# Optimization experiments

Measured on AMD Instinct MI355X. Metric: run time of the kernel, lower is better.

The kernel has to match this reference:

```python
import jax, jax.numpy as jnp
import numpy as np

HOPS = 2
BN_EPS = 1e-5


def _glorot(key, shape):
    fan_in = shape[-2]
    bound = 1.0 / np.sqrt(fan_in)
    return jax.random.uniform(key, shape, jnp.float32, -bound, bound)


def setup_inputs() -> dict:
    key = jax.random.key(0)
    ks = jax.random.split(key, 12)
    n, e = 50000, 800000
    in_c, hid, out_c = 128, 96, 64
    x = jax.random.normal(ks[0], (n, in_c), jnp.float32)
    edge_index = jax.random.randint(ks[1], (2, e), 0, n, jnp.int32)
    # MixHopLayer 0: hops+1 linears in_c -> hid (stacked)
    conv0_W = _glorot(ks[2], (HOPS + 1, in_c, hid))
    conv0_b = jnp.zeros((HOPS + 1, hid), jnp.float32)
    # MixHopLayer 1: hops+1 linears hid*(hops+1) -> out_c
    conv1_W = _glorot(ks[3], (HOPS + 1, hid * (HOPS + 1), out_c))
    conv1_b = jnp.zeros((HOPS + 1, out_c), jnp.float32)
    # BatchNorm1d(hid*(hops+1)) eval-mode params/buffers
    w = hid * (HOPS + 1)
    bn_gamma = jnp.ones((w,), jnp.float32)
    bn_beta = jnp.zeros((w,), jnp.float32)
    bn_mean = 0.1 * jax.random.normal(ks[4], (w,), jnp.float32)
    bn_var = jnp.ones((w,), jnp.float32) + 0.1 * jax.random.uniform(ks[5], (w,))
    # final projection out_c*(hops+1) -> out_c
    fp_W = _glorot(ks[6], (out_c * (HOPS + 1), out_c))
    fp_b = jnp.zeros((out_c,), jnp.float32)
    return dict(x=x, edge_index=edge_index, conv0_W=conv0_W, conv0_b=conv0_b,
                conv1_W=conv1_W, conv1_b=conv1_b, bn_gamma=bn_gamma, bn_beta=bn_beta,
                bn_mean=bn_mean, bn_var=bn_var, fp_W=fp_W, fp_b=fp_b)


def _gcn_norm(edge_index, n):
    # PyG gcn_norm with add_self_loops=True, improved=False, symmetric norm.
    row, col = edge_index[0], edge_index[1]
    loop = jnp.arange(n, dtype=edge_index.dtype)
    row = jnp.concatenate([row, loop])
    col = jnp.concatenate([col, loop])
    deg = jax.ops.segment_sum(jnp.ones_like(col, jnp.float32), col, num_segments=n)
    dinv = jnp.where(deg > 0, jax.lax.rsqrt(deg), 0.0)
    w = dinv[row] * dinv[col]
    return row, col, w


def _spmm_adj_t(row, col, w, x, n):
    # adj_t = SparseTensor(row=col, col=row, value=w): out[col] += w * x[row]
    return jax.ops.segment_sum(w[:, None] * x[row], col, num_segments=n)


def _mixhop_layer(x, W, b, row, col, w, n):
    xs = [x @ W[0] + b[0]]
    for j in range(1, HOPS + 1):
        xj = x @ W[j] + b[j]
        for _ in range(j):
            xj = _spmm_adj_t(row, col, w, xj, n)
        xs.append(xj)
    return jnp.concatenate(xs, axis=1)


def reference(x, edge_index, conv0_W, conv0_b, conv1_W, conv1_b,
              bn_gamma, bn_beta, bn_mean, bn_var, fp_W, fp_b):
    n = x.shape[0]
    row, col, w = _gcn_norm(edge_index, n)
    h = _mixhop_layer(x, conv0_W, conv0_b, row, col, w, n)
    # BatchNorm1d (eval) + ReLU; dropout is identity in eval
    h = bn_gamma * (h - bn_mean) * jax.lax.rsqrt(bn_var + BN_EPS) + bn_beta
    h = jax.nn.relu(h)
    h = _mixhop_layer(h, conv1_W, conv1_b, row, col, w, n)
    return h @ fp_W + fp_b
```

## Files before the change

### kernel.cpp

```cpp
#include <hip/hip_runtime.h>

#define IN_C 128
#define HID 96
#define OUT_C 64
#define W0C 288
#define W1C 192
#define CAP 5120
#define EPB 4096

typedef __bf16 bf16x8v __attribute__((ext_vector_type(8)));
typedef float  f32x4v  __attribute__((ext_vector_type(4)));


__global__ void k_zero(int* __restrict__ p, int n) {
    int i = blockIdx.x * blockDim.x + threadIdx.x;
    if (i < n) p[i] = 0;
}

__global__ void k_count(const int* __restrict__ col, int* __restrict__ counts, int e) {
    int i = blockIdx.x * blockDim.x + threadIdx.x;
    if (i < e) atomicAdd(&counts[col[i]], 1);
}

__global__ void k_block_sum(const int* __restrict__ counts, int* __restrict__ bsums,
                            float* __restrict__ dinv, int n) {
    __shared__ int s[256];
    int i = blockIdx.x * 256 + threadIdx.x;
    int v = (i < n) ? counts[i] : 0;
    if (i < n) dinv[i] = rsqrtf((float)(v + 1));
    s[threadIdx.x] = v;
    __syncthreads();
    for (int off = 128; off > 0; off >>= 1) {
        if (threadIdx.x < (unsigned)off) s[threadIdx.x] += s[threadIdx.x + off];
        __syncthreads();
    }
    if (threadIdx.x == 0) bsums[blockIdx.x] = s[0];
}

__global__ void k_scan_bsums(int* __restrict__ bsums, int nb) {
    __shared__ int s[256];
    int v = ((int)threadIdx.x < nb) ? bsums[threadIdx.x] : 0;
    s[threadIdx.x] = v;
    __syncthreads();
    for (int off = 1; off < 256; off <<= 1) {
        int t = ((int)threadIdx.x >= off) ? s[threadIdx.x - off] : 0;
        __syncthreads();
        s[threadIdx.x] += t;
        __syncthreads();
    }
    if ((int)threadIdx.x < nb) bsums[threadIdx.x] = s[threadIdx.x] - v;
}

__global__ void k_row_ptr(const int* __restrict__ counts, const int* __restrict__ boffs,
                          int* __restrict__ row_ptr, int n) {
    __shared__ int s[256];
    int i = blockIdx.x * 256 + threadIdx.x;
    int v = (i < n) ? counts[i] : 0;
    s[threadIdx.x] = v;
    __syncthreads();
    for (int off = 1; off < 256; off <<= 1) {
        int t = ((int)threadIdx.x >= off) ? s[threadIdx.x - off] : 0;
        __syncthreads();
        s[threadIdx.x] += t;
        __syncthreads();
    }
    if (i < n) {
        row_ptr[i] = boffs[blockIdx.x] + s[threadIdx.x] - v;
        if (i == n - 1) row_ptr[n] = boffs[blockIdx.x] + s[threadIdx.x];
    }
}

__global__ __launch_bounds__(256) void k_binscatter(
        const int* __restrict__ row, const int* __restrict__ col,
        const int* __restrict__ row_ptr, int* __restrict__ bcur ,
        int2* __restrict__ binned, int e) {
    __shared__ int hist[256];
    __shared__ int base[256];
    int tid = threadIdx.x;
    int e0 = blockIdx.x * EPB;
    int cnt = min(EPB, e - e0);
    hist[tid] = 0;
    __syncthreads();
    int rr[16], cc[16], rk[16];
#pragma unroll
    for (int k = 0; k < 16; k++) {
        int idx = tid + k * 256;
        if (idx < cnt) {
            rr[k] = row[e0 + idx];
            cc[k] = col[e0 + idx];
            rk[k] = atomicAdd(&hist[cc[k] >> 8], 1);
        }
    }
    __syncthreads();
    {
        int h = hist[tid];
        if (h > 0) base[tid] = atomicAdd(&bcur[tid * 16], h);
    }
    __syncthreads();
#pragma unroll
    for (int k = 0; k < 16; k++) {
        int idx = tid + k * 256;
        if (idx < cnt) {
            int b = cc[k] >> 8;
            binned[row_ptr[b << 8] + base[b] + rk[k]] = make_int2(rr[k], cc[k]);
        }
    }
}

__global__ __launch_bounds__(256) void k_bucket_sort(
        const int2* __restrict__ binned, const int* __restrict__ row_ptr,
        const float* __restrict__ dinv,
        int* __restrict__ csr_src, float* __restrict__ csr_w,
        float* __restrict__ arow, int n) {
    __shared__ int   s_src[CAP];
    __shared__ int   s_col[CAP];
    __shared__ int   s_ofs[256];
    __shared__ int   lcur[256];
    __shared__ float s_a[256];
    int tid = threadIdx.x;
    int node0 = blockIdx.x << 8;
    int nodeEnd = min(node0 + 256, n);
    int base = row_ptr[node0];
    int end  = row_ptr[nodeEnd];
    int cnt  = end - base;

    lcur[tid] = 0;
    __syncthreads();
    for (int t = tid; t < cnt; t += 256) {
        atomicAdd(&lcur[binned[base + t].x >> 8], 1);
    }
    __syncthreads();
    {
        int v = lcur[tid];
        s_ofs[tid] = v;
        __syncthreads();
        for (int o = 1; o < 256; o <<= 1) {
            int u = (tid >= o) ? s_ofs[tid - o] : 0;
            __syncthreads();
            s_ofs[tid] += u;
            __syncthreads();
        }
        lcur[tid] = s_ofs[tid] - v;
    }
    __syncthreads();
    for (int t = tid; t < cnt; t += 256) {
        int2 rc = binned[base + t];
        int pos = atomicAdd(&lcur[rc.x >> 8], 1);
        if (pos < CAP) {
            s_src[pos] = rc.x;
            s_col[pos] = rc.y;
        }
    }
    __syncthreads();
    {
        int node = node0 + tid;
        s_ofs[tid] = (node < n) ? (row_ptr[node] - base) : cnt;
        lcur[tid] = 0;
        s_a[tid] = 0.f;
    }
    __syncthreads();
    int lim = min(cnt, CAP);
    for (int t = tid; t < lim; t += 256) {
        int r = s_src[t], c = s_col[t];
        int local = c - node0;
        int pos = s_ofs[local] + atomicAdd(&lcur[local], 1);
        float wv = dinv[r] * dinv[c];
        csr_src[base + pos] = r;
        csr_w[base + pos]   = wv;
        atomicAdd(&s_a[local], wv);
    }
    __syncthreads();
    {
        int node = node0 + tid;
        if (node < n) {
            float d = dinv[node];
            arow[node] = s_a[tid] + d * d;
        }
    }
}


__global__ void k_cvt_bf16(const float* __restrict__ src, __bf16* __restrict__ dst, int n8) {
    int i = blockIdx.x * blockDim.x + threadIdx.x;
    if (i >= n8) return;
    bf16x8v o;
#pragma unroll
    for (int q = 0; q < 8; q++) o[q] = (__bf16)src[i * 8 + q];
    *(bf16x8v*)(dst + (size_t)i * 8) = o;
}

__global__ void k_prep_all(const float* __restrict__ W0, const float* __restrict__ W1,
                           const float* __restrict__ Wf,
                           const float* __restrict__ gamma, const float* __restrict__ beta,
                           const float* __restrict__ mean, const float* __restrict__ var,
                           __bf16* __restrict__ w0t, __bf16* __restrict__ w1t,
                           __bf16* __restrict__ wft,
                           float* __restrict__ scale, float* __restrict__ shift) {
    const int T0 = 3 * IN_C * HID;
    const int T1 = 3 * W0C * OUT_C;
    const int T2 = W1C * OUT_C;
    int i = blockIdx.x * blockDim.x + threadIdx.x;
    if (i < T0) {
        int kn = IN_C * HID;
        int j = i / kn, r = i % kn;
        int k = r / HID, nn = r % HID;
        w0t[(size_t)j * kn + (size_t)nn * IN_C + k] = (__bf16)W0[i];
    } else if (i < T0 + T1) {
        int ii = i - T0;
        int kn = W0C * OUT_C;
        int j = ii / kn, r = ii % kn;
        int k = r / OUT_C, nn = r % OUT_C;
        w1t[(size_t)j * kn + (size_t)nn * W0C + k] = (__bf16)W1[ii];
    } else if (i < T0 + T1 + T2) {
        int ii = i - T0 - T1;
        int k = ii / OUT_C, nn = ii % OUT_C;
        wft[(size_t)nn * W1C + k] = (__bf16)Wf[ii];
    } else if (i < T0 + T1 + T2 + W0C) {
        int ii = i - T0 - T1 - T2;
        float s = gamma[ii] * rsqrtf(var[ii] + 1e-5f);
        scale[ii] = s;
        shift[ii] = beta[ii] - mean[ii] * s;
    }
}


__global__ __launch_bounds__(256) void k_mf_l0a(
        const __bf16* __restrict__ xb, const __bf16* __restrict__ w0t ,
        const float* __restrict__ bias ,
        __bf16* __restrict__ h,
        const float* __restrict__ scale, const float* __restrict__ shift, int M) {
    const int RS = 104;
    __shared__ __bf16 tile[128 * RS];
    int tid = threadIdx.x;
    int wave = tid >> 6, lane = tid & 63;
    int ln = lane & 15, quad = lane >> 4;
    int rowBase = blockIdx.x * 128;
    int waveRow = wave * 16;
    f32x4v acc[2][6];
#pragma unroll
    for (int u = 0; u < 2; u++)
#pragma unroll
        for (int t = 0; t < 6; t++) acc[u][t] = (f32x4v){0.f, 0.f, 0.f, 0.f};
    const __bf16* arow0 = xb + (size_t)(rowBase + waveRow + ln) * IN_C + quad * 8;
    const __bf16* arow1 = arow0 + (size_t)64 * IN_C;
#pragma unroll
    for (int k = 0; k < 4; k++) {
        bf16x8v a0 = *(const bf16x8v*)(arow0 + k * 32);
        bf16x8v a1 = *(const bf16x8v*)(arow1 + k * 32);
#pragma unroll
        for (int c = 0; c < 6; c++) {
            bf16x8v b = *(const bf16x8v*)(w0t + (size_t)(c * 16 + ln) * IN_C + k * 32 + quad * 8);
            acc[0][c] = __builtin_amdgcn_mfma_f32_16x16x32_bf16(a0, b, acc[0][c], 0, 0, 0);
            acc[1][c] = __builtin_amdgcn_mfma_f32_16x16x32_bf16(a1, b, acc[1][c], 0, 0, 0);
        }
    }
#pragma unroll
    for (int u = 0; u < 2; u++)
#pragma unroll
        for (int r = 0; r < 4; r++) {
            int lr = u * 64 + waveRow + quad * 4 + r;
#pragma unroll
            for (int c = 0; c < 6; c++) {
                int col = c * 16 + ln;
                float v = acc[u][c][r] + bias[col];
                v = fmaxf(v * scale[col] + shift[col], 0.f);
                tile[lr * RS + col] = (__bf16)v;
            }
        }
    __syncthreads();
#pragma unroll
    for (int s = 0; s < 6; s++) {
        int idx = tid + s * 256;
        int r = idx / 12, c8 = idx % 12;
        int grow = rowBase + r;
        if (grow < M)
            *(bf16x8v*)(h + (size_t)grow * W0C + c8 * 8) =
                *(const bf16x8v*)(tile + r * RS + c8 * 8);
    }
}

__global__ __launch_bounds__(256) void k_mf_l0b(
        const __bf16* __restrict__ s1, const __bf16* __restrict__ w0t,
        const float* __restrict__ bias , const float* __restrict__ arow,
        __bf16* __restrict__ h, __bf16* __restrict__ tp,
        const float* __restrict__ scale, const float* __restrict__ shift, int M) {
    const int RS = 104;
    __shared__ __bf16 tile[128 * RS];
    int tid = threadIdx.x;
    int wave = tid >> 6, lane = tid & 63;
    int ln = lane & 15, quad = lane >> 4;
    int rowBase = blockIdx.x * 128;
    int waveRow = wave * 16;
    const __bf16* w1p = w0t + (size_t)1 * HID * IN_C;
    const __bf16* w2p = w0t + (size_t)2 * HID * IN_C;
    f32x4v acc[2][2][6];
#pragma unroll
    for (int j = 0; j < 2; j++)
#pragma unroll
        for (int u = 0; u < 2; u++)
#pragma unroll
            for (int t = 0; t < 6; t++) acc[j][u][t] = (f32x4v){0.f, 0.f, 0.f, 0.f};
    const __bf16* arow0 = s1 + (size_t)(rowBase + waveRow + ln) * IN_C + quad * 8;
    const __bf16* arow1 = arow0 + (size_t)64 * IN_C;
#pragma unroll
    for (int k = 0; k < 4; k++) {
        bf16x8v a0 = *(const bf16x8v*)(arow0 + k * 32);
        bf16x8v a1 = *(const bf16x8v*)(arow1 + k * 32);
#pragma unroll
        for (int c = 0; c < 6; c++) {
            bf16x8v b1 = *(const bf16x8v*)(w1p + (size_t)(c * 16 + ln) * IN_C + k * 32 + quad * 8);
            bf16x8v b2 = *(const bf16x8v*)(w2p + (size_t)(c * 16 + ln) * IN_C + k * 32 + quad * 8);
            acc[0][0][c] = __builtin_amdgcn_mfma_f32_16x16x32_bf16(a0, b1, acc[0][0][c], 0, 0, 0);
            acc[0][1][c] = __builtin_amdgcn_mfma_f32_16x16x32_bf16(a1, b1, acc[0][1][c], 0, 0, 0);
            acc[1][0][c] = __builtin_amdgcn_mfma_f32_16x16x32_bf16(a0, b2, acc[1][0][c], 0, 0, 0);
            acc[1][1][c] = __builtin_amdgcn_mfma_f32_16x16x32_bf16(a1, b2, acc[1][1][c], 0, 0, 0);
        }
    }
    float avs[2][4];
#pragma unroll
    for (int u = 0; u < 2; u++)
#pragma unroll
        for (int r = 0; r < 4; r++)
            avs[u][r] = arow[rowBase + u * 64 + waveRow + quad * 4 + r];
#pragma unroll
    for (int jj = 0; jj < 2; jj++) {
        const float* bj = bias + (jj + 1) * HID;
#pragma unroll
        for (int u = 0; u < 2; u++)
#pragma unroll
            for (int r = 0; r < 4; r++) {
                int lr = u * 64 + waveRow + quad * 4 + r;
                float av = avs[u][r];
#pragma unroll
                for (int c = 0; c < 6; c++) {
                    int col = c * 16 + ln;
                    float v = acc[jj][u][c][r] + av * bj[col];
                    if (jj == 0) v = fmaxf(v * scale[HID + col] + shift[HID + col], 0.f);
                    tile[lr * RS + col] = (__bf16)v;
                }
            }
        __syncthreads();
#pragma unroll
        for (int s = 0; s < 6; s++) {
            int idx = tid + s * 256;
            int r = idx / 12, c8 = idx % 12;
            int grow = rowBase + r;
            if (grow < M) {
                __bf16* dst = (jj == 0) ? (h + (size_t)grow * W0C + HID)
                                        : (tp + (size_t)grow * HID);
                *(bf16x8v*)(dst + c8 * 8) = *(const bf16x8v*)(tile + r * RS + c8 * 8);
            }
        }
        __syncthreads();
    }
}

__global__ __launch_bounds__(256) void k_mf_l1m(
        const __bf16* __restrict__ hb, const __bf16* __restrict__ w1t ,
        const float* __restrict__ bias ,
        __bf16* __restrict__ g, __bf16* __restrict__ u12, int M) {
    const int RS = 72;
    __shared__ __bf16 tile[128 * RS];
    int tid = threadIdx.x;
    int wave = tid >> 6, lane = tid & 63;
    int ln = lane & 15, quad = lane >> 4;
    int rowBase = blockIdx.x * 128;
    int waveRow = wave * 16;
    f32x4v acc[3][2][4];
#pragma unroll
    for (int j = 0; j < 3; j++)
#pragma unroll
        for (int u = 0; u < 2; u++)
#pragma unroll
            for (int t = 0; t < 4; t++) acc[j][u][t] = (f32x4v){0.f, 0.f, 0.f, 0.f};
    const __bf16* arow0 = hb + (size_t)(rowBase + waveRow + ln) * W0C + quad * 8;
    const __bf16* arow1 = arow0 + (size_t)64 * W0C;
#pragma unroll
    for (int k = 0; k < 9; k++) {
        bf16x8v a0 = *(const bf16x8v*)(arow0 + k * 32);
        bf16x8v a1 = *(const bf16x8v*)(arow1 + k * 32);
#pragma unroll
        for (int c = 0; c < 4; c++) {
#pragma unroll
            for (int j = 0; j < 3; j++) {
                bf16x8v b = *(const bf16x8v*)(w1t + (size_t)j * OUT_C * W0C +
                                              (size_t)(c * 16 + ln) * W0C + k * 32 + quad * 8);
                acc[j][0][c] = __builtin_amdgcn_mfma_f32_16x16x32_bf16(a0, b, acc[j][0][c], 0, 0, 0);
                acc[j][1][c] = __builtin_amdgcn_mfma_f32_16x16x32_bf16(a1, b, acc[j][1][c], 0, 0, 0);
            }
        }
    }
#pragma unroll
    for (int j = 0; j < 3; j++) {
        const float* bj = bias + j * OUT_C;
#pragma unroll
        for (int u = 0; u < 2; u++)
#pragma unroll
            for (int r = 0; r < 4; r++) {
                int lr = u * 64 + waveRow + quad * 4 + r;
#pragma unroll
                for (int c = 0; c < 4; c++) {
                    int col = c * 16 + ln;
                    tile[lr * RS + col] = (__bf16)(acc[j][u][c][r] + bj[col]);
                }
            }
        __syncthreads();
        __bf16* dst = (j == 0) ? g : u12;
        int ld = (j == 0) ? W1C : 128;
        int c0 = (j == 2) ? OUT_C : 0;
#pragma unroll
        for (int s = 0; s < 4; s++) {
            int idx = tid + s * 256;
            int r = idx / 8, c8 = idx % 8;
            int grow = rowBase + r;
            if (grow < M)
                *(bf16x8v*)(dst + (size_t)grow * ld + c0 + c8 * 8) =
                    *(const bf16x8v*)(tile + r * RS + c8 * 8);
        }
        __syncthreads();
    }
}

__global__ __launch_bounds__(256) void k_mf_fin(
        const __bf16* __restrict__ gb, const __bf16* __restrict__ wft ,
        const float* __restrict__ bias, float* __restrict__ out, int M) {
    const int RS = 68;
    __shared__ float tile[128 * RS];
    int tid = threadIdx.x;
    int wave = tid >> 6, lane = tid & 63;
    int ln = lane & 15, quad = lane >> 4;
    int rowBase = blockIdx.x * 128;
    int waveRow = wave * 16;
    f32x4v acc[2][4];
#pragma unroll
    for (int u = 0; u < 2; u++)
#pragma unroll
        for (int t = 0; t < 4; t++) acc[u][t] = (f32x4v){0.f, 0.f, 0.f, 0.f};
    const __bf16* arow0 = gb + (size_t)(rowBase + waveRow + ln) * W1C + quad * 8;
    const __bf16* arow1 = arow0 + (size_t)64 * W1C;
#pragma unroll
    for (int k = 0; k < 6; k++) {
        bf16x8v a0 = *(const bf16x8v*)(arow0 + k * 32);
        bf16x8v a1 = *(const bf16x8v*)(arow1 + k * 32);
#pragma unroll
        for (int c = 0; c < 4; c++) {
            bf16x8v b = *(const bf16x8v*)(wft + (size_t)(c * 16 + ln) * W1C + k * 32 + quad * 8);
            acc[0][c] = __builtin_amdgcn_mfma_f32_16x16x32_bf16(a0, b, acc[0][c], 0, 0, 0);
            acc[1][c] = __builtin_amdgcn_mfma_f32_16x16x32_bf16(a1, b, acc[1][c], 0, 0, 0);
        }
    }
#pragma unroll
    for (int u = 0; u < 2; u++)
#pragma unroll
        for (int r = 0; r < 4; r++) {
            int lr = u * 64 + waveRow + quad * 4 + r;
#pragma unroll
            for (int c = 0; c < 4; c++) {
                int col = c * 16 + ln;
                tile[lr * RS + col] = acc[u][c][r] + bias[col];
            }
        }
    __syncthreads();
#pragma unroll
    for (int s = 0; s < 8; s++) {
        int idx = tid + s * 256;
        int r = idx / 16, c4 = idx % 16;
        int grow = rowBase + r;
        if (grow < M)
            *(float4*)(out + (size_t)grow * OUT_C + c4 * 4) =
                *(const float4*)(tile + r * RS + c4 * 4);
    }
}

template <int C8, int NPB, bool BNRELU>
__global__ void k_spmm(const __bf16* __restrict__ xin, int ldx,
                       __bf16* __restrict__ xout, int ldo,
                       const int* __restrict__ row_ptr, const int* __restrict__ counts,
                       const int* __restrict__ csr_src, const float* __restrict__ csr_w,
                       const float* __restrict__ dinv, int n,
                       const float* __restrict__ scale, const float* __restrict__ shift,
                       int chan0) {
    int c8 = threadIdx.x % C8;
    int nl = threadIdx.x / C8;
    int node = blockIdx.x * NPB + nl;
    if (node >= n) return;
    float di = dinv[node];
    float lw = di * di;
    float acc[8];
    {
        bf16x8v v = *(const bf16x8v*)(xin + (size_t)node * ldx + c8 * 8);
#pragma unroll
        for (int q = 0; q < 8; q++) acc[q] = lw * (float)v[q];
    }
    int start = row_ptr[node];
    int cnt = counts[node];
    int k = 0;
    for (; k + 4 <= cnt; k += 4) {
        int s0 = csr_src[start + k + 0], s1 = csr_src[start + k + 1];
        int s2 = csr_src[start + k + 2], s3 = csr_src[start + k + 3];
        float w0 = csr_w[start + k + 0], w1 = csr_w[start + k + 1];
        float w2 = csr_w[start + k + 2], w3 = csr_w[start + k + 3];
        bf16x8v v0 = *(const bf16x8v*)(xin + (size_t)s0 * ldx + c8 * 8);
        bf16x8v v1 = *(const bf16x8v*)(xin + (size_t)s1 * ldx + c8 * 8);
        bf16x8v v2 = *(const bf16x8v*)(xin + (size_t)s2 * ldx + c8 * 8);
        bf16x8v v3 = *(const bf16x8v*)(xin + (size_t)s3 * ldx + c8 * 8);
#pragma unroll
        for (int q = 0; q < 8; q++)
            acc[q] += w0 * (float)v0[q] + w1 * (float)v1[q] +
                      w2 * (float)v2[q] + w3 * (float)v3[q];
    }
    for (; k < cnt; k++) {
        int src = csr_src[start + k];
        float w = csr_w[start + k];
        bf16x8v xv = *(const bf16x8v*)(xin + (size_t)src * ldx + c8 * 8);
#pragma unroll
        for (int q = 0; q < 8; q++) acc[q] += w * (float)xv[q];
    }
    bf16x8v o;
#pragma unroll
    for (int q = 0; q < 8; q++) {
        float v = acc[q];
        if (BNRELU) {
            int ch = chan0 + c8 * 8 + q;
            v = fmaxf(v * scale[ch] + shift[ch], 0.f);
        }
        o[q] = (__bf16)v;
    }
    *(bf16x8v*)(xout + (size_t)node * ldo + c8 * 8) = o;
}

template <int C8, int SPLIT, int NPB, bool BNA, bool BNB>
__global__ void k_spmm2(const __bf16* __restrict__ xin, int ldx,
                        __bf16* __restrict__ dstA, int ldA, int chanA,
                        __bf16* __restrict__ dstB, int ldB, int chanB,
                        const int* __restrict__ row_ptr, const int* __restrict__ counts,
                        const int* __restrict__ csr_src, const float* __restrict__ csr_w,
                        const float* __restrict__ dinv, int n,
                        const float* __restrict__ scale, const float* __restrict__ shift) {
    int c8 = threadIdx.x % C8;
    int nl = threadIdx.x / C8;
    int node = blockIdx.x * NPB + nl;
    if (node >= n) return;
    float di = dinv[node];
    float lw = di * di;
    float acc[8];
    {
        bf16x8v v = *(const bf16x8v*)(xin + (size_t)node * ldx + c8 * 8);
#pragma unroll
        for (int q = 0; q < 8; q++) acc[q] = lw * (float)v[q];
    }
    int start = row_ptr[node];
    int cnt = counts[node];
    int k = 0;
    for (; k + 4 <= cnt; k += 4) {
        int s0 = csr_src[start + k + 0], s1 = csr_src[start + k + 1];
        int s2 = csr_src[start + k + 2], s3 = csr_src[start + k + 3];
        float w0 = csr_w[start + k + 0], w1 = csr_w[start + k + 1];
        float w2 = csr_w[start + k + 2], w3 = csr_w[start + k + 3];
        bf16x8v v0 = *(const bf16x8v*)(xin + (size_t)s0 * ldx + c8 * 8);
        bf16x8v v1 = *(const bf16x8v*)(xin + (size_t)s1 * ldx + c8 * 8);
        bf16x8v v2 = *(const bf16x8v*)(xin + (size_t)s2 * ldx + c8 * 8);
        bf16x8v v3 = *(const bf16x8v*)(xin + (size_t)s3 * ldx + c8 * 8);
#pragma unroll
        for (int q = 0; q < 8; q++)
            acc[q] += w0 * (float)v0[q] + w1 * (float)v1[q] +
                      w2 * (float)v2[q] + w3 * (float)v3[q];
    }
    for (; k < cnt; k++) {
        int src = csr_src[start + k];
        float w = csr_w[start + k];
        bf16x8v xv = *(const bf16x8v*)(xin + (size_t)src * ldx + c8 * 8);
#pragma unroll
        for (int q = 0; q < 8; q++) acc[q] += w * (float)xv[q];
    }
    bool isA = c8 < SPLIT;
    __bf16* dst = isA ? dstA : dstB;
    int ld   = isA ? ldA : ldB;
    int lc8  = isA ? c8 : c8 - SPLIT;
    int chan = isA ? chanA : chanB;
    bool bn  = isA ? BNA : BNB;
    bf16x8v o;
#pragma unroll
    for (int q = 0; q < 8; q++) {
        float v = acc[q];
        if (bn) {
            int ch = chan + lc8 * 8 + q;
            v = fmaxf(v * scale[ch] + shift[ch], 0.f);
        }
        o[q] = (__bf16)v;
    }
    *(bf16x8v*)(dst + (size_t)node * ld + lc8 * 8) = o;
}


extern "C" void kernel_launch(void* const* d_in, const int* in_sizes, int n_in,
                              void* d_out, int out_size, void* d_ws, size_t ws_size,
                              hipStream_t stream) {
    const int n = in_sizes[0] / IN_C;
    const int e = in_sizes[1] / 2;

    const float* x    = (const float*)d_in[0];
    const int*   ei   = (const int*)d_in[1];
    const float* W0   = (const float*)d_in[2];
    const float* b0   = (const float*)d_in[3];
    const float* W1   = (const float*)d_in[4];
    const float* b1   = (const float*)d_in[5];
    const float* bn_g = (const float*)d_in[6];
    const float* bn_b = (const float*)d_in[7];
    const float* bn_m = (const float*)d_in[8];
    const float* bn_v = (const float*)d_in[9];
    const float* Wf   = (const float*)d_in[10];
    const float* bf   = (const float*)d_in[11];
    float* out = (float*)d_out;

    const int* e_row = ei;
    const int* e_col = ei + e;

    char* ws = (char*)d_ws;
    size_t off = 0;
    auto alloc = [&](size_t bytes) -> void* {
        void* p = ws + off;
        off += (bytes + 255) & ~(size_t)255;
        return p;
    };
    const int NP = n + 128;
    int*    counts  = (int*)alloc((size_t)(n + 256 * 16) * 4);
    int*    bcur    = counts + n;
    int*    row_ptr = (int*)alloc((size_t)(n + 1) * 4);
    int*    bsums   = (int*)alloc(256 * 4);
    float*  dinv    = (float*)alloc((size_t)n * 4);
    float*  arow    = (float*)alloc((size_t)NP * 4);
    int2*   binned  = (int2*)alloc((size_t)e * 8);
    int*    csr_src = (int*)alloc((size_t)e * 4);
    float*  csr_w   = (float*)alloc((size_t)e * 4);
    float*  bnscale = (float*)alloc(W0C * 4);
    float*  bnshift = (float*)alloc(W0C * 4);
    __bf16* xb  = (__bf16*)alloc((size_t)NP * IN_C * 2);
    __bf16* w0t = (__bf16*)alloc((size_t)3 * HID * IN_C * 2);
    __bf16* w1t = (__bf16*)alloc((size_t)3 * OUT_C * W0C * 2);
    __bf16* wft = (__bf16*)alloc((size_t)OUT_C * W1C * 2);
    __bf16* s1  = (__bf16*)alloc((size_t)NP * 128 * 2);
    __bf16* tp  = (__bf16*)alloc((size_t)NP * HID * 2);
    __bf16* h   = (__bf16*)alloc((size_t)NP * W0C * 2);
    __bf16* g   = (__bf16*)alloc((size_t)NP * W1C * 2);
    __bf16* u12 = s1;
    __bf16* up  = tp;

    const int TB = 256;
    int nb = (n + 255) / 256;

    k_zero<<<dim3((n + 256 * 16 + TB - 1) / TB), dim3(TB), 0, stream>>>(counts, n + 256 * 16);
    k_count<<<dim3((e + TB - 1) / TB), dim3(TB), 0, stream>>>(e_col, counts, e);
    k_block_sum<<<dim3(nb), dim3(256), 0, stream>>>(counts, bsums, dinv, n);
    k_scan_bsums<<<dim3(1), dim3(256), 0, stream>>>(bsums, nb);
    k_row_ptr<<<dim3(nb), dim3(256), 0, stream>>>(counts, bsums, row_ptr, n);
    k_binscatter<<<dim3((e + EPB - 1) / EPB), dim3(256), 0, stream>>>(e_row, e_col, row_ptr,
                                                                      bcur, binned, e);
    k_bucket_sort<<<dim3(nb), dim3(256), 0, stream>>>(binned, row_ptr, dinv,
                                                      csr_src, csr_w, arow, n);

    k_cvt_bf16<<<dim3((n * IN_C / 8 + TB - 1) / TB), dim3(TB), 0, stream>>>(x, xb, n * IN_C / 8);
    int ptotal = 3 * IN_C * HID + 3 * W0C * OUT_C + W1C * OUT_C + W0C;
    k_prep_all<<<dim3((ptotal + TB - 1) / TB), dim3(TB), 0, stream>>>(
        W0, W1, Wf, bn_g, bn_b, bn_m, bn_v, w0t, w1t, wft, bnscale, bnshift);

    dim3 g128((n + 127) / 128);

    k_mf_l0a<<<g128, dim3(256), 0, stream>>>(xb, w0t, b0, h, bnscale, bnshift, n);
    k_spmm<16, 16, false><<<dim3((n + 15) / 16), dim3(256), 0, stream>>>(
        xb, IN_C, s1, 128, row_ptr, counts, csr_src, csr_w, dinv, n,
        nullptr, nullptr, 0);
    k_mf_l0b<<<g128, dim3(256), 0, stream>>>(s1, w0t, b0, arow, h, tp, bnscale, bnshift, n);
    k_spmm<12, 16, true><<<dim3((n + 15) / 16), dim3(192), 0, stream>>>(
        tp, HID, h + 2 * HID, W0C, row_ptr, counts, csr_src, csr_w, dinv, n,
        bnscale, bnshift, 2 * HID);

    k_mf_l1m<<<g128, dim3(256), 0, stream>>>(h, w1t, b1, g, u12, n);

    k_spmm2<16, 8, 16, false, false><<<dim3((n + 15) / 16), dim3(256), 0, stream>>>(
        u12, 128, g + OUT_C, W1C, 0, up, OUT_C, 0,
        row_ptr, counts, csr_src, csr_w, dinv, n, nullptr, nullptr);
    k_spmm<8, 32, false><<<dim3((n + 31) / 32), dim3(256), 0, stream>>>(
        up, OUT_C, g + 2 * OUT_C, W1C, row_ptr, counts, csr_src, csr_w, dinv, n,
        nullptr, nullptr, 0);

    k_mf_fin<<<g128, dim3(256), 0, stream>>>(g, wft, bf, out, n);
}
```

Measured before the change: 354.4 us.

## Merge prep kernels, overlap edge counting with layer-0 GEMM, shrink GEMM tiles

Three prep launches (x-to-bf16 conversion, weight transpose/BN fold, counter zeroing) become one kernel that dispatches on block index. The edge-degree atomic count now runs as extra blocks inside the first layer-0 GEMM launch, so the two overlap and launch overhead drops. The l0b and l1m GEMMs move from 128-row to 64-row tiles, which doubles the block count and halves per-thread accumulators, trading B-operand reuse for occupancy. Reordering puts the l0a GEMM before CSR construction; it depends only on xb and the prep outputs, so this stays valid.

```diff
diff --git a/kernel.cpp b/kernel.cpp
--- a/kernel.cpp
+++ b/kernel.cpp
@@ -11,16 +11,6 @@
 typedef __bf16 bf16x8v __attribute__((ext_vector_type(8)));
 typedef float  f32x4v  __attribute__((ext_vector_type(4)));
 
-
-__global__ void k_zero(int* __restrict__ p, int n) {
-    int i = blockIdx.x * blockDim.x + threadIdx.x;
-    if (i < n) p[i] = 0;
-}
-
-__global__ void k_count(const int* __restrict__ col, int* __restrict__ counts, int e) {
-    int i = blockIdx.x * blockDim.x + threadIdx.x;
-    if (i < e) atomicAdd(&counts[col[i]], 1);
-}
 
 __global__ void k_block_sum(const int* __restrict__ counts, int* __restrict__ bsums,
                             float* __restrict__ dinv, int n) {
@@ -179,58 +169,70 @@
     }
 }
 
-
-__global__ void k_cvt_bf16(const float* __restrict__ src, __bf16* __restrict__ dst, int n8) {
-    int i = blockIdx.x * blockDim.x + threadIdx.x;
-    if (i >= n8) return;
-    bf16x8v o;
-#pragma unroll
-    for (int q = 0; q < 8; q++) o[q] = (__bf16)src[i * 8 + q];
-    *(bf16x8v*)(dst + (size_t)i * 8) = o;
-}
-
-__global__ void k_prep_all(const float* __restrict__ W0, const float* __restrict__ W1,
-                           const float* __restrict__ Wf,
-                           const float* __restrict__ gamma, const float* __restrict__ beta,
-                           const float* __restrict__ mean, const float* __restrict__ var,
-                           __bf16* __restrict__ w0t, __bf16* __restrict__ w1t,
-                           __bf16* __restrict__ wft,
-                           float* __restrict__ scale, float* __restrict__ shift) {
-    const int T0 = 3 * IN_C * HID;
-    const int T1 = 3 * W0C * OUT_C;
-    const int T2 = W1C * OUT_C;
-    int i = blockIdx.x * blockDim.x + threadIdx.x;
-    if (i < T0) {
-        int kn = IN_C * HID;
-        int j = i / kn, r = i % kn;
-        int k = r / HID, nn = r % HID;
-        w0t[(size_t)j * kn + (size_t)nn * IN_C + k] = (__bf16)W0[i];
-    } else if (i < T0 + T1) {
-        int ii = i - T0;
-        int kn = W0C * OUT_C;
-        int j = ii / kn, r = ii % kn;
-        int k = r / OUT_C, nn = r % OUT_C;
-        w1t[(size_t)j * kn + (size_t)nn * W0C + k] = (__bf16)W1[ii];
-    } else if (i < T0 + T1 + T2) {
-        int ii = i - T0 - T1;
-        int k = ii / OUT_C, nn = ii % OUT_C;
-        wft[(size_t)nn * W1C + k] = (__bf16)Wf[ii];
-    } else if (i < T0 + T1 + T2 + W0C) {
-        int ii = i - T0 - T1 - T2;
-        float s = gamma[ii] * rsqrtf(var[ii] + 1e-5f);
-        scale[ii] = s;
-        shift[ii] = beta[ii] - mean[ii] * s;
-    }
-}
-
-
-__global__ __launch_bounds__(256) void k_mf_l0a(
+__global__ void k_combo_prep(const float* __restrict__ x, __bf16* __restrict__ xb, int n8,
+                             const float* __restrict__ W0, const float* __restrict__ W1,
+                             const float* __restrict__ Wf,
+                             const float* __restrict__ gamma, const float* __restrict__ beta,
+                             const float* __restrict__ mean, const float* __restrict__ var,
+                             __bf16* __restrict__ w0t, __bf16* __restrict__ w1t,
+                             __bf16* __restrict__ wft,
+                             float* __restrict__ scale, float* __restrict__ shift,
+                             int* __restrict__ zp, int nz,
+                             int CB, int PB) {
+    int b = blockIdx.x;
+    if (b < CB) {
+        int i = b * 256 + threadIdx.x;
+        if (i >= n8) return;
+        bf16x8v o;
+#pragma unroll
+        for (int q = 0; q < 8; q++) o[q] = (__bf16)x[i * 8 + q];
+        *(bf16x8v*)(xb + (size_t)i * 8) = o;
+    } else if (b < CB + PB) {
+        const int T0 = 3 * IN_C * HID;
+        const int T1 = 3 * W0C * OUT_C;
+        const int T2 = W1C * OUT_C;
+        int i = (b - CB) * 256 + threadIdx.x;
+        if (i < T0) {
+            int kn = IN_C * HID;
+            int j = i / kn, r = i % kn;
+            int k = r / HID, nn = r % HID;
+            w0t[(size_t)j * kn + (size_t)nn * IN_C + k] = (__bf16)W0[i];
+        } else if (i < T0 + T1) {
+            int ii = i - T0;
+            int kn = W0C * OUT_C;
+            int j = ii / kn, r = ii % kn;
+            int k = r / OUT_C, nn = r % OUT_C;
+            w1t[(size_t)j * kn + (size_t)nn * W0C + k] = (__bf16)W1[ii];
+        } else if (i < T0 + T1 + T2) {
+            int ii = i - T0 - T1;
+            int k = ii / OUT_C, nn = ii % OUT_C;
+            wft[(size_t)nn * W1C + k] = (__bf16)Wf[ii];
+        } else if (i < T0 + T1 + T2 + W0C) {
+            int ii = i - T0 - T1 - T2;
+            float s = gamma[ii] * rsqrtf(var[ii] + 1e-5f);
+            scale[ii] = s;
+            shift[ii] = beta[ii] - mean[ii] * s;
+        }
+    } else {
+        int i = (b - CB - PB) * 256 + threadIdx.x;
+        if (i < nz) zp[i] = 0;
+    }
+}
+
+
+__global__ __launch_bounds__(256) void k_count_l0a(
+        const int* __restrict__ col, int* __restrict__ counts, int e,
         const __bf16* __restrict__ xb, const __bf16* __restrict__ w0t ,
         const float* __restrict__ bias ,
         __bf16* __restrict__ h,
-        const float* __restrict__ scale, const float* __restrict__ shift, int M) {
+        const float* __restrict__ scale, const float* __restrict__ shift, int M, int GG) {
     const int RS = 104;
     __shared__ __bf16 tile[128 * RS];
+    if ((int)blockIdx.x >= GG) {
+        int i = (blockIdx.x - GG) * 256 + threadIdx.x;
+        if (i < e) atomicAdd(&counts[col[i]], 1);
+        return;
+    }
     int tid = threadIdx.x;
     int wave = tid >> 6, lane = tid & 63;
     int ln = lane & 15, quad = lane >> 4;
@@ -261,10 +263,10 @@
             int lr = u * 64 + waveRow + quad * 4 + r;
 #pragma unroll
             for (int c = 0; c < 6; c++) {
-                int col = c * 16 + ln;
-                float v = acc[u][c][r] + bias[col];
-                v = fmaxf(v * scale[col] + shift[col], 0.f);
-                tile[lr * RS + col] = (__bf16)v;
+                int col2 = c * 16 + ln;
+                float v = acc[u][c][r] + bias[col2];
+                v = fmaxf(v * scale[col2] + shift[col2], 0.f);
+                tile[lr * RS + col2] = (__bf16)v;
             }
         }
     __syncthreads();
@@ -285,63 +287,53 @@
         __bf16* __restrict__ h, __bf16* __restrict__ tp,
         const float* __restrict__ scale, const float* __restrict__ shift, int M) {
     const int RS = 104;
-    __shared__ __bf16 tile[128 * RS];
+    __shared__ __bf16 tile[64 * RS];
     int tid = threadIdx.x;
     int wave = tid >> 6, lane = tid & 63;
     int ln = lane & 15, quad = lane >> 4;
-    int rowBase = blockIdx.x * 128;
+    int rowBase = blockIdx.x * 64;
     int waveRow = wave * 16;
     const __bf16* w1p = w0t + (size_t)1 * HID * IN_C;
     const __bf16* w2p = w0t + (size_t)2 * HID * IN_C;
-    f32x4v acc[2][2][6];
+    f32x4v acc[2][6];
 #pragma unroll
     for (int j = 0; j < 2; j++)
 #pragma unroll
-        for (int u = 0; u < 2; u++)
-#pragma unroll
-            for (int t = 0; t < 6; t++) acc[j][u][t] = (f32x4v){0.f, 0.f, 0.f, 0.f};
+        for (int t = 0; t < 6; t++) acc[j][t] = (f32x4v){0.f, 0.f, 0.f, 0.f};
     const __bf16* arow0 = s1 + (size_t)(rowBase + waveRow + ln) * IN_C + quad * 8;
-    const __bf16* arow1 = arow0 + (size_t)64 * IN_C;
 #pragma unroll
     for (int k = 0; k < 4; k++) {
         bf16x8v a0 = *(const bf16x8v*)(arow0 + k * 32);
-        bf16x8v a1 = *(const bf16x8v*)(arow1 + k * 32);
 #pragma unroll
         for (int c = 0; c < 6; c++) {
             bf16x8v b1 = *(const bf16x8v*)(w1p + (size_t)(c * 16 + ln) * IN_C + k * 32 + quad * 8);
             bf16x8v b2 = *(const bf16x8v*)(w2p + (size_t)(c * 16 + ln) * IN_C + k * 32 + quad * 8);
-            acc[0][0][c] = __builtin_amdgcn_mfma_f32_16x16x32_bf16(a0, b1, acc[0][0][c], 0, 0, 0);
-            acc[0][1][c] = __builtin_amdgcn_mfma_f32_16x16x32_bf16(a1, b1, acc[0][1][c], 0, 0, 0);
-            acc[1][0][c] = __builtin_amdgcn_mfma_f32_16x16x32_bf16(a0, b2, acc[1][0][c], 0, 0, 0);
-            acc[1][1][c] = __builtin_amdgcn_mfma_f32_16x16x32_bf16(a1, b2, acc[1][1][c], 0, 0, 0);
-        }
-    }
-    float avs[2][4];
-#pragma unroll
-    for (int u = 0; u < 2; u++)
-#pragma unroll
-        for (int r = 0; r < 4; r++)
-            avs[u][r] = arow[rowBase + u * 64 + waveRow + quad * 4 + r];
+            acc[0][c] = __builtin_amdgcn_mfma_f32_16x16x32_bf16(a0, b1, acc[0][c], 0, 0, 0);
+            acc[1][c] = __builtin_amdgcn_mfma_f32_16x16x32_bf16(a0, b2, acc[1][c], 0, 0, 0);
+        }
+    }
+    float avs[4];
+#pragma unroll
+    for (int r = 0; r < 4; r++)
+        avs[r] = arow[rowBase + waveRow + quad * 4 + r];
 #pragma unroll
     for (int jj = 0; jj < 2; jj++) {
         const float* bj = bias + (jj + 1) * HID;
 #pragma unroll
-        for (int u = 0; u < 2; u++)
-#pragma unroll
-            for (int r = 0; r < 4; r++) {
-                int lr = u * 64 + waveRow + quad * 4 + r;
-                float av = avs[u][r];
-#pragma unroll
-                for (int c = 0; c < 6; c++) {
-                    int col = c * 16 + ln;
-                    float v = acc[jj][u][c][r] + av * bj[col];
-                    if (jj == 0) v = fmaxf(v * scale[HID + col] + shift[HID + col], 0.f);
-                    tile[lr * RS + col] = (__bf16)v;
-                }
+        for (int r = 0; r < 4; r++) {
+            int lr = waveRow + quad * 4 + r;
+            float av = avs[r];
+#pragma unroll
+            for (int c = 0; c < 6; c++) {
+                int col = c * 16 + ln;
+                float v = acc[jj][c][r] + av * bj[col];
+                if (jj == 0) v = fmaxf(v * scale[HID + col] + shift[HID + col], 0.f);
+                tile[lr * RS + col] = (__bf16)v;
             }
-        __syncthreads();
-#pragma unroll
-        for (int s = 0; s < 6; s++) {
+        }
+        __syncthreads();
+#pragma unroll
+        for (int s = 0; s < 3; s++) {
             int idx = tid + s * 256;
             int r = idx / 12, c8 = idx % 12;
             int grow = rowBase + r;
@@ -360,33 +352,28 @@
         const float* __restrict__ bias ,
         __bf16* __restrict__ g, __bf16* __restrict__ u12, int M) {
     const int RS = 72;
-    __shared__ __bf16 tile[128 * RS];
+    __shared__ __bf16 tile[64 * RS];
     int tid = threadIdx.x;
     int wave = tid >> 6, lane = tid & 63;
     int ln = lane & 15, quad = lane >> 4;
-    int rowBase = blockIdx.x * 128;
+    int rowBase = blockIdx.x * 64;
     int waveRow = wave * 16;
-    f32x4v acc[3][2][4];
+    f32x4v acc[3][4];
 #pragma unroll
     for (int j = 0; j < 3; j++)
 #pragma unroll
-        for (int u = 0; u < 2; u++)
-#pragma unroll
-            for (int t = 0; t < 4; t++) acc[j][u][t] = (f32x4v){0.f, 0.f, 0.f, 0.f};
+        for (int t = 0; t < 4; t++) acc[j][t] = (f32x4v){0.f, 0.f, 0.f, 0.f};
     const __bf16* arow0 = hb + (size_t)(rowBase + waveRow + ln) * W0C + quad * 8;
-    const __bf16* arow1 = arow0 + (size_t)64 * W0C;
 #pragma unroll
     for (int k = 0; k < 9; k++) {
         bf16x8v a0 = *(const bf16x8v*)(arow0 + k * 32);
-        bf16x8v a1 = *(const bf16x8v*)(arow1 + k * 32);
 #pragma unroll
         for (int c = 0; c < 4; c++) {
 #pragma unroll
             for (int j = 0; j < 3; j++) {
                 bf16x8v b = *(const bf16x8v*)(w1t + (size_t)j * OUT_C * W0C +
                                               (size_t)(c * 16 + ln) * W0C + k * 32 + quad * 8);
-                acc[j][0][c] = __builtin_amdgcn_mfma_f32_16x16x32_bf16(a0, b, acc[j][0][c], 0, 0, 0);
-                acc[j][1][c] = __builtin_amdgcn_mfma_f32_16x16x32_bf16(a1, b, acc[j][1][c], 0, 0, 0);
+                acc[j][c] = __builtin_amdgcn_mfma_f32_16x16x32_bf16(a0, b, acc[j][c], 0, 0, 0);
             }
         }
     }
@@ -394,22 +381,20 @@
     for (int j = 0; j < 3; j++) {
         const float* bj = bias + j * OUT_C;
 #pragma unroll
-        for (int u = 0; u < 2; u++)
-#pragma unroll
-            for (int r = 0; r < 4; r++) {
-                int lr = u * 64 + waveRow + quad * 4 + r;
-#pragma unroll
-                for (int c = 0; c < 4; c++) {
-                    int col = c * 16 + ln;
-                    tile[lr * RS + col] = (__bf16)(acc[j][u][c][r] + bj[col]);
-                }
+        for (int r = 0; r < 4; r++) {
+            int lr = waveRow + quad * 4 + r;
+#pragma unroll
+            for (int c = 0; c < 4; c++) {
+                int col = c * 16 + ln;
+                tile[lr * RS + col] = (__bf16)(acc[j][c][r] + bj[col]);
             }
+        }
         __syncthreads();
         __bf16* dst = (j == 0) ? g : u12;
         int ld = (j == 0) ? W1C : 128;
         int c0 = (j == 2) ? OUT_C : 0;
 #pragma unroll
-        for (int s = 0; s < 4; s++) {
+        for (int s = 0; s < 2; s++) {
             int idx = tid + s * 256;
             int r = idx / 8, c8 = idx % 8;
             int grow = rowBase + r;
@@ -646,11 +631,23 @@
     __bf16* u12 = s1;
     __bf16* up  = tp;
 
-    const int TB = 256;
     int nb = (n + 255) / 256;
 
-    k_zero<<<dim3((n + 256 * 16 + TB - 1) / TB), dim3(TB), 0, stream>>>(counts, n + 256 * 16);
-    k_count<<<dim3((e + TB - 1) / TB), dim3(TB), 0, stream>>>(e_col, counts, e);
+    int n8 = n * IN_C / 8;
+    int nz = n + 256 * 16;
+    int ptotal = 3 * IN_C * HID + 3 * W0C * OUT_C + W1C * OUT_C + W0C;
+    int CB = (n8 + 255) / 256;
+    int PB = (ptotal + 255) / 256;
+    int ZB = (nz + 255) / 256;
+    k_combo_prep<<<dim3(CB + PB + ZB), dim3(256), 0, stream>>>(
+        x, xb, n8, W0, W1, Wf, bn_g, bn_b, bn_m, bn_v,
+        w0t, w1t, wft, bnscale, bnshift, counts, nz, CB, PB);
+
+    int GG = (n + 127) / 128;
+    int EB = (e + 255) / 256;
+    k_count_l0a<<<dim3(GG + EB), dim3(256), 0, stream>>>(
+        e_col, counts, e, xb, w0t, b0, h, bnscale, bnshift, n, GG);
+
     k_block_sum<<<dim3(nb), dim3(256), 0, stream>>>(counts, bsums, dinv, n);
     k_scan_bsums<<<dim3(1), dim3(256), 0, stream>>>(bsums, nb);
     k_row_ptr<<<dim3(nb), dim3(256), 0, stream>>>(counts, bsums, row_ptr, n);
@@ -659,23 +656,17 @@
     k_bucket_sort<<<dim3(nb), dim3(256), 0, stream>>>(binned, row_ptr, dinv,
                                                       csr_src, csr_w, arow, n);
 
-    k_cvt_bf16<<<dim3((n * IN_C / 8 + TB - 1) / TB), dim3(TB), 0, stream>>>(x, xb, n * IN_C / 8);
-    int ptotal = 3 * IN_C * HID + 3 * W0C * OUT_C + W1C * OUT_C + W0C;
-    k_prep_all<<<dim3((ptotal + TB - 1) / TB), dim3(TB), 0, stream>>>(
-        W0, W1, Wf, bn_g, bn_b, bn_m, bn_v, w0t, w1t, wft, bnscale, bnshift);
-
-    dim3 g128((n + 127) / 128);
-
-    k_mf_l0a<<<g128, dim3(256), 0, stream>>>(xb, w0t, b0, h, bnscale, bnshift, n);
+    dim3 g64((n + 63) / 64);
+
     k_spmm<16, 16, false><<<dim3((n + 15) / 16), dim3(256), 0, stream>>>(
         xb, IN_C, s1, 128, row_ptr, counts, csr_src, csr_w, dinv, n,
         nullptr, nullptr, 0);
-    k_mf_l0b<<<g128, dim3(256), 0, stream>>>(s1, w0t, b0, arow, h, tp, bnscale, bnshift, n);
+    k_mf_l0b<<<g64, dim3(256), 0, stream>>>(s1, w0t, b0, arow, h, tp, bnscale, bnshift, n);
     k_spmm<12, 16, true><<<dim3((n + 15) / 16), dim3(192), 0, stream>>>(
         tp, HID, h + 2 * HID, W0C, row_ptr, counts, csr_src, csr_w, dinv, n,
         bnscale, bnshift, 2 * HID);
 
-    k_mf_l1m<<<g128, dim3(256), 0, stream>>>(h, w1t, b1, g, u12, n);
+    k_mf_l1m<<<g64, dim3(256), 0, stream>>>(h, w1t, b1, g, u12, n);
 
     k_spmm2<16, 8, 16, false, false><<<dim3((n + 15) / 16), dim3(256), 0, stream>>>(
         u12, 128, g + OUT_C, W1C, 0, up, OUT_C, 0,
@@ -684,5 +675,5 @@
         up, OUT_C, g + 2 * OUT_C, W1C, row_ptr, counts, csr_src, csr_w, dinv, n,
         nullptr, nullptr, 0);
 
-    k_mf_fin<<<g128, dim3(256), 0, stream>>>(g, wft, bf, out, n);
-}
+    k_mf_fin<<<dim3((n + 127) / 128), dim3(256), 0, stream>>>(g, wft, bf, out, n);
+}
```

New measurement: 342.9 us. 3.2% less time.
